# Kernel tuning notes

Measured on AMD Instinct MI355X. Metric: run time of the kernel, lower is better.

The kernel has to match this reference:

```python
import jax, jax.numpy as jnp
import numpy as np

N_HEADS = 8
EPS = 1e-5


def setup_inputs() -> dict:
    key = jax.random.key(0)
    ks = jax.random.split(key, 5)
    c = 512
    x = jax.random.normal(ks[0], (2, c, 2, 32, 32), dtype=jnp.float32)
    s = 0.02
    Wq = jax.random.normal(ks[1], (c, c), dtype=jnp.float32) * s
    Wk = jax.random.normal(ks[2], (c, c), dtype=jnp.float32) * s
    Wv = jax.random.normal(ks[3], (c, c), dtype=jnp.float32) * s
    Wo = jax.random.normal(ks[4], (c, c), dtype=jnp.float32) * s
    bo = jnp.zeros((c,), dtype=jnp.float32)
    gamma = jnp.ones((c,), dtype=jnp.float32)
    beta = jnp.zeros((c,), dtype=jnp.float32)
    return {"x": x, "Wq": Wq, "Wk": Wk, "Wv": Wv, "Wo": Wo, "bo": bo,
            "gamma": gamma, "beta": beta}


def reference(x, Wq, Wk, Wv, Wo, bo, gamma, beta):
    b, c, d, h, w = x.shape
    seq = d * h * w
    # [b, c, d, h, w] -> [b, seq, c]
    xs = jnp.transpose(x, (0, 2, 3, 4, 1)).reshape(b, seq, c)
    # LayerNorm over channel dim
    mu = jnp.mean(xs, axis=-1, keepdims=True)
    var = jnp.mean(jnp.square(xs - mu), axis=-1, keepdims=True)
    xn = (xs - mu) * jax.lax.rsqrt(var + EPS) * gamma + beta
    # Self-attention (cond falls back to x); weights stored [in, out]
    dh = c // N_HEADS
    q = (xn @ Wq).reshape(b, seq, N_HEADS, dh)
    k = (xn @ Wk).reshape(b, seq, N_HEADS, dh)
    v = (xn @ Wv).reshape(b, seq, N_HEADS, dh)
    scale = dh ** (-0.5)
    attn = jnp.einsum('bihd,bjhd->bhij', q, k) * scale  # [b, H, seq, seq]
    attn = jax.nn.softmax(attn, axis=-1)
    out = jnp.einsum('bhij,bjhd->bihd', attn, v).reshape(b, seq, c)
    out = out @ Wo + bo
    y = out + xs  # residual
    return jnp.transpose(y.reshape(b, d, h, w, c), (0, 4, 1, 2, 3))
```

## Files before the change

### kernel.cpp

```cpp
#include <hip/hip_runtime.h>
#include <cstdint>
#include <cstring>

typedef unsigned short u16;
typedef unsigned char u8;
typedef __bf16 bf16x8 __attribute__((ext_vector_type(8)));
typedef float f32x4 __attribute__((ext_vector_type(4)));
typedef u16 u16x4 __attribute__((ext_vector_type(4)));
typedef u16 u16x8 __attribute__((ext_vector_type(8)));
typedef long l64x2 __attribute__((ext_vector_type(2)));

__device__ __forceinline__ u16 f2bf(float f) {
  union { float f; unsigned u; } v; v.f = f;
  unsigned r = v.u + 0x7FFFu + ((v.u >> 16) & 1u);
  return (u16)(r >> 16);
}

__device__ __forceinline__ float bf2f(u16 u) {
  union { unsigned u; float f; } c; c.u = ((unsigned)u) << 16;
  return c.f;
}

__device__ __forceinline__ f32x4 mfma16(bf16x8 a, bf16x8 b, f32x4 c) {
  return __builtin_amdgcn_mfma_f32_16x16x32_bf16(a, b, c, 0, 0, 0);
}

__device__ __forceinline__ f32x4 mfma8(long a, long b, f32x4 c) {
  return __builtin_amdgcn_mfma_f32_16x16x32_fp8_fp8(a, b, c, 0, 0, 0);
}

__device__ __forceinline__ u8 f2fp8(float f) {
  return (u8)(__builtin_amdgcn_cvt_pk_fp8_f32(f, f, 0, false) & 0xff);
}

__device__ __forceinline__ void gload_lds16(const void* g, void* l) {
  auto* lp = reinterpret_cast<__attribute__((address_space(3))) unsigned int*>(
      reinterpret_cast<uintptr_t>(l));
  const auto* gp = reinterpret_cast<const __attribute__((address_space(1))) unsigned int*>(
      reinterpret_cast<uintptr_t>(g));
  __builtin_amdgcn_global_load_lds(gp, lp, 16, 0, 0);
}

template <int N>
__device__ __forceinline__ void waitcnt_vm() {
  if constexpr (N == 0)      asm volatile("s_waitcnt vmcnt(0)" ::: "memory");
  else if constexpr (N == 2) asm volatile("s_waitcnt vmcnt(2)" ::: "memory");
  else if constexpr (N == 4) asm volatile("s_waitcnt vmcnt(4)" ::: "memory");
  else if constexpr (N == 6) asm volatile("s_waitcnt vmcnt(6)" ::: "memory");
  else                       asm volatile("s_waitcnt vmcnt(8)" ::: "memory");
}

__global__ __launch_bounds__(256) void prep_kernel(const float* __restrict__ Wq,
                                                   const float* __restrict__ Wk,
                                                   const float* __restrict__ Wv,
                                                   const float* __restrict__ Wo,
                                                   const float* __restrict__ x,
                                                   const float* __restrict__ gamma,
                                                   const float* __restrict__ beta,
                                                   u8* __restrict__ wt8f,
                                                   u16* __restrict__ wtWo,
                                                   u8* __restrict__ xn8f) {
  struct LnSh {
    float red0[16][16];
    float red1[16][16];
    float mu[16], rs[16];
    u8 tile8[16][520];
  };
  struct WtSh { float tile[32][33]; };
  __shared__ __align__(16) char shraw[sizeof(LnSh) > sizeof(WtSh) ? sizeof(LnSh) : sizeof(WtSh)];
  int bid = blockIdx.x;
  int t = threadIdx.x;
  if (bid < 256) {
    LnSh& S = *reinterpret_cast<LnSh*>(shraw);
    int b = bid >> 7;
    int s0 = (bid & 127) * 16;
    int tx = t & 15, ty = t >> 4;
    const float* xb = x + (size_t)b * 512 * 2048 + s0 + tx;
    float vals[32];
    float sum = 0.f, sq = 0.f;
#pragma unroll
    for (int k = 0; k < 32; k++) {
      float v = xb[(size_t)(ty + k * 16) * 2048];
      vals[k] = v;
      sum += v; sq += v * v;
    }
    S.red0[ty][tx] = sum; S.red1[ty][tx] = sq;
    __syncthreads();
    if (t < 16) {
      float a = 0.f, c2 = 0.f;
#pragma unroll
      for (int i = 0; i < 16; i++) { a += S.red0[i][t]; c2 += S.red1[i][t]; }
      float mu = a * (1.f / 512.f);
      float var = c2 * (1.f / 512.f) - mu * mu;
      S.mu[t] = mu;
      S.rs[t] = rsqrtf(var + 1e-5f);
    }
    __syncthreads();
    float mu = S.mu[tx], rs = S.rs[tx];
#pragma unroll
    for (int k = 0; k < 32; k++) {
      int ch = ty + k * 16;
      S.tile8[tx][ch] = f2fp8((vals[k] - mu) * rs * gamma[ch] + beta[ch]);
    }
    __syncthreads();
    int lrow2 = t & 15, kt = t >> 4;
    int grow = b * 2048 + s0;
    int rt2 = grow >> 5;
    int ihalf = (s0 >> 4) & 1;
    u8* dst = xn8f + ((size_t)rt2 * 16 + kt) * 1024 + ihalf * 8;
#pragma unroll
    for (int kg = 0; kg < 4; kg++) {
      unsigned long long v;
      memcpy(&v, &S.tile8[lrow2][kt * 32 + kg * 8], 8);
      *(unsigned long long*)(dst + (size_t)(lrow2 + kg * 16) * 16) = v;
    }
  } else {
    WtSh& S = *reinterpret_cast<WtSh*>(shraw);
    int wid = bid - 256;
    int z = wid >> 8;
    const float* W = (z == 0) ? Wq : (z == 1) ? Wk : (z == 2) ? Wv : Wo;
    int rem = wid & 255;
    int n0 = (rem >> 4) * 32, k0 = (rem & 15) * 32;
    int tx = t & 31, ty = t >> 5;
#pragma unroll
    for (int i = 0; i < 4; i++)
      S.tile[ty + i * 8][tx] = W[(size_t)(k0 + ty + i * 8) * 512 + n0 + tx];
    __syncthreads();
    if (z < 3) {
      if (t < 128) {
        int lane = t >> 1, jhalf = t & 1;
        int nn = (lane & 15) + jhalf * 16;
        int kk0 = (lane >> 4) * 8;
        u8 pk[8];
#pragma unroll
        for (int j = 0; j < 8; j++) pk[j] = f2fp8(S.tile[kk0 + j][nn]);
        unsigned long long v;
        memcpy(&v, pk, 8);
        size_t addr = (size_t)z * 262144 + ((size_t)(n0 >> 5) * 16 + (k0 >> 5)) * 1024 +
                      (size_t)lane * 16 + jhalf * 8;
        *(unsigned long long*)(wt8f + addr) = v;
      }
    } else {
#pragma unroll
      for (int i = 0; i < 4; i++) {
        int n = ty + i * 8;
        wtWo[(size_t)(n0 + n) * 512 + k0 + tx] = f2bf(S.tile[tx][n]);
      }
    }
  }
}

template <int AM, int AN>
__device__ __forceinline__ void gemm_tile_ring(const u16* __restrict__ A, const u16* __restrict__ B,
                                               int m0, int n0, f32x4 acc[AM][AN],
                                               u16* As, u16* Bs) {
  constexpr int BM = AM * 32, BN = AN * 32;
  constexpr int LA = BM / 64, LB = BN / 64;
  constexpr int L = LA + LB;
  int t = threadIdx.x;
  int w = t >> 6, lane = t & 63;
  int wm = w >> 1, wn = w & 1;
  int arow = t >> 2;
  int acol = (t & 3) * 8;
  int lrow = lane & 15;
  int lko = (lane >> 4) * 8;

  auto stage = [&](int buf, int k0) {
#pragma unroll
    for (int g = 0; g < LA; ++g)
      gload_lds16(A + (size_t)(m0 + g * 64 + arow) * 512 + k0 + acol,
                  As + buf * (BM * 32) + g * 2048 + w * 512);
#pragma unroll
    for (int g = 0; g < LB; ++g)
      gload_lds16(B + (size_t)(n0 + g * 64 + arow) * 512 + k0 + acol,
                  Bs + buf * (BN * 32) + g * 2048 + w * 512);
  };

  stage(0, 0);
  stage(1, 32);
  stage(2, 64);
  __syncthreads();

  for (int tt = 0; tt < 16; ++tt) {
    int pk = (tt + 3 < 16) ? (tt + 3) * 32 : 0;
    stage((tt + 3) & 3, pk);
    const u16* as = As + (tt & 3) * (BM * 32);
    const u16* bs = Bs + (tt & 3) * (BN * 32);
    bf16x8 af[AM], bfr[AN];
#pragma unroll
    for (int i = 0; i < AM; i++) af[i] = *(const bf16x8*)(as + (wm * (AM * 16) + i * 16 + lrow) * 32 + lko);
#pragma unroll
    for (int j = 0; j < AN; j++) bfr[j] = *(const bf16x8*)(bs + (wn * (AN * 16) + j * 16 + lrow) * 32 + lko);
    __builtin_amdgcn_s_setprio(1);
#pragma unroll
    for (int i = 0; i < AM; i++)
#pragma unroll
      for (int j = 0; j < AN; j++)
        acc[i][j] = mfma16(af[i], bfr[j], acc[i][j]);
    __builtin_amdgcn_s_setprio(0);
    waitcnt_vm<2 * L>();
    __builtin_amdgcn_s_barrier();
  }
  waitcnt_vm<0>();
}

__global__ __launch_bounds__(256, 4) void gemm_qkv(const u8* __restrict__ xn8f, const u8* __restrict__ wt8f,
                                                   u8* __restrict__ Qb, u8* __restrict__ Kp,
                                                   u8* __restrict__ Vp) {
  const float SCQ = 0.125f * 1.4426950408889634f;
  int mat = blockIdx.z;
  int bx = blockIdx.x, by = blockIdx.y;
  int t = threadIdx.x, w = t >> 6, lane = t & 63;
  int lrow = lane & 15, lgrp = lane >> 4;

  const u8* Af = xn8f + (size_t)(bx * 4 + w) * 16384 + (size_t)lane * 16;
  const u8* Bf = wt8f + (size_t)mat * 262144 + (size_t)(by * 2) * 16384 + (size_t)lane * 16;

  f32x4 acc[2][4] = {};
  long aA[2], bA[4], aB[2], bB[4];

  auto loadAB = [&](long* a, long* bb, int kt) {
    l64x2 av = *(const l64x2*)(Af + kt * 1024);
    l64x2 b0 = *(const l64x2*)(Bf + kt * 1024);
    l64x2 b1 = *(const l64x2*)(Bf + 16384 + kt * 1024);
    a[0] = av[0]; a[1] = av[1];
    bb[0] = b0[0]; bb[1] = b0[1]; bb[2] = b1[0]; bb[3] = b1[1];
  };
  auto step = [&](const long* a, const long* bb) {
    __builtin_amdgcn_s_setprio(1);
#pragma unroll
    for (int i = 0; i < 2; i++)
#pragma unroll
      for (int j = 0; j < 4; j++)
        acc[i][j] = mfma8(a[i], bb[j], acc[i][j]);
    __builtin_amdgcn_s_setprio(0);
  };

  loadAB(aA, bA, 0);
  for (int kt = 0; kt < 16; kt += 2) {
    loadAB(aB, bB, (kt + 1) & 15);
    step(aA, bA);
    loadAB(aA, bA, (kt + 2) & 15);
    step(aB, bB);
  }

#pragma unroll
  for (int i = 0; i < 2; i++) {
#pragma unroll
    for (int j = 0; j < 4; j++) {
      int gr0 = bx * 128 + w * 32 + i * 16 + lgrp * 4;
      int gc = by * 64 + j * 16 + lrow;
      if (mat == 0) {
#pragma unroll
        for (int r = 0; r < 4; r++)
          Qb[(size_t)(gr0 + r) * 512 + gc] = f2fp8(acc[i][j][r] * SCQ);
      } else if (mat == 1) {
        int h = gc >> 6, d = gc & 63;
        int half = d >> 5, lg = (d >> 3) & 3, jj = d & 7;
#pragma unroll
        for (int r = 0; r < 4; r++) {
          int kg = gr0 + r;
          int bq = kg >> 11, kl = kg & 2047;
          int kt2 = kl >> 5, kw = kl & 31;
          int tt = (kw >> 2) & 1;
          int kwb = kw - 4 * tt;
          int lr = ((kwb >> 3) << 2) | (kwb & 3);
          size_t idx = (size_t)((bq * 8 + h) * 64 + kt2) * 2048 + tt * 1024 +
                       (lg * 16 + lr) * 16 + half * 8 + jj;
          Kp[idx] = f2fp8(acc[i][j][r]);
        }
      } else {
        int h = gc >> 6, d = gc & 63;
        int dt = d >> 4, lr = d & 15;
        int kg = gr0;
        int bq = kg >> 11, kl = kg & 2047;
        int kt2 = kl >> 5, kw = kl & 31;
        int lg = kw >> 3, j0 = kw & 7;
        unsigned u = __builtin_amdgcn_cvt_pk_fp8_f32(acc[i][j][0], acc[i][j][1], 0, false);
        u = __builtin_amdgcn_cvt_pk_fp8_f32(acc[i][j][2], acc[i][j][3], u, true);
        size_t idx = (size_t)((bq * 8 + h) * 64 + kt2) * 2048 + (dt >> 1) * 1024 +
                     (lg * 16 + lr) * 16 + (dt & 1) * 8 + j0;
        *(unsigned*)(Vp + idx) = u;
      }
    }
  }
}

__global__ __launch_bounds__(256, 4) void attn_kernel(const u8* __restrict__ Qb, const u8* __restrict__ Kp,
                                                      const u8* __restrict__ Vp, u16* __restrict__ Opart,
                                                      float* __restrict__ ml, int logS) {
  const long ONES8 = 0x3838383838383838L;
  int S = 1 << logS;
  int bid = blockIdx.x;
  int qt = bid >> (4 + logS);
  int group = bid & (16 * S - 1);
  int hb = group >> logS, sp = group & (S - 1);
  int b = hb >> 3, h = hb & 7;
  int kt0 = sp * (64 >> logS);
  int nsteps = 64 >> logS;

  int t = threadIdx.x, w = t >> 6, lane = t & 63;
  int lrow = lane & 15, lgrp = lane >> 4, lko = lgrp * 8;
  int q0 = qt * 128 + w * 32;

  const u8* Qp = Qb + (size_t)(b * 2048 + q0 + lrow) * 512 + h * 64 + lko;
  long qa0 = *(const long*)(Qp);
  long qa1 = *(const long*)(Qp + 32);
  long qb0 = *(const long*)(Qp + 16 * 512);
  long qb1 = *(const long*)(Qp + 16 * 512 + 32);

  const u8* Kbh = Kp + (size_t)hb * 131072 + lane * 16;
  const u8* Vbh = Vp + (size_t)hb * 131072 + lane * 16;

  f32x4 acca[4] = {}, accb[4] = {};
  f32x4 suma = {}, sumb = {};

  long kA[4], vA[4], kB[4], vB[4];

  auto loadKV = [&](long* kf, long* vf, int st) {
    const u8* pk = Kbh + (size_t)(kt0 + st) * 2048;
    const u8* pv = Vbh + (size_t)(kt0 + st) * 2048;
    l64x2 a0 = *(const l64x2*)(pk);
    l64x2 a1 = *(const l64x2*)(pk + 1024);
    l64x2 b0 = *(const l64x2*)(pv);
    l64x2 b1 = *(const l64x2*)(pv + 1024);
    kf[0] = a0[0]; kf[1] = a0[1]; kf[2] = a1[0]; kf[3] = a1[1];
    vf[0] = b0[0]; vf[1] = b0[1]; vf[2] = b1[0]; vf[3] = b1[1];
  };

  auto computeStep = [&](const long* kc, const long* vc) {
    f32x4 sa0 = {}, sa1 = {}, sb0 = {}, sb1 = {};
    __builtin_amdgcn_s_setprio(1);
    sa0 = mfma8(kc[0], qa0, sa0);
    sa0 = mfma8(kc[1], qa1, sa0);
    sa1 = mfma8(kc[2], qa0, sa1);
    sa1 = mfma8(kc[3], qa1, sa1);
    sb0 = mfma8(kc[0], qb0, sb0);
    sb0 = mfma8(kc[1], qb1, sb0);
    sb1 = mfma8(kc[2], qb0, sb1);
    sb1 = mfma8(kc[3], qb1, sb1);
    __builtin_amdgcn_s_setprio(0);

    float pa[8], pb8[8];
#pragma unroll
    for (int jj = 0; jj < 4; jj++) pa[jj] = exp2f(sa0[jj]);
#pragma unroll
    for (int jj = 0; jj < 4; jj++) pa[4 + jj] = exp2f(sa1[jj]);
#pragma unroll
    for (int jj = 0; jj < 4; jj++) pb8[jj] = exp2f(sb0[jj]);
#pragma unroll
    for (int jj = 0; jj < 4; jj++) pb8[4 + jj] = exp2f(sb1[jj]);

    unsigned alo = __builtin_amdgcn_cvt_pk_fp8_f32(pa[0], pa[1], 0, false);
    alo = __builtin_amdgcn_cvt_pk_fp8_f32(pa[2], pa[3], alo, true);
    unsigned ahi = __builtin_amdgcn_cvt_pk_fp8_f32(pa[4], pa[5], 0, false);
    ahi = __builtin_amdgcn_cvt_pk_fp8_f32(pa[6], pa[7], ahi, true);
    long pla = (long)(((unsigned long long)ahi << 32) | alo);
    unsigned blo = __builtin_amdgcn_cvt_pk_fp8_f32(pb8[0], pb8[1], 0, false);
    blo = __builtin_amdgcn_cvt_pk_fp8_f32(pb8[2], pb8[3], blo, true);
    unsigned bhi = __builtin_amdgcn_cvt_pk_fp8_f32(pb8[4], pb8[5], 0, false);
    bhi = __builtin_amdgcn_cvt_pk_fp8_f32(pb8[6], pb8[7], bhi, true);
    long plb = (long)(((unsigned long long)bhi << 32) | blo);

    __builtin_amdgcn_s_setprio(1);
    acca[0] = mfma8(pla, vc[0], acca[0]);
    acca[1] = mfma8(pla, vc[1], acca[1]);
    acca[2] = mfma8(pla, vc[2], acca[2]);
    acca[3] = mfma8(pla, vc[3], acca[3]);
    accb[0] = mfma8(plb, vc[0], accb[0]);
    accb[1] = mfma8(plb, vc[1], accb[1]);
    accb[2] = mfma8(plb, vc[2], accb[2]);
    accb[3] = mfma8(plb, vc[3], accb[3]);
    suma = mfma8(pla, ONES8, suma);
    sumb = mfma8(plb, ONES8, sumb);
    __builtin_amdgcn_s_setprio(0);
  };

  loadKV(kA, vA, 0);
  for (int st = 0; st < nsteps; st += 2) {
    loadKV(kB, vB, (st + 1 < nsteps) ? st + 1 : 0);
    computeStep(kA, vA);
    loadKV(kA, vA, (st + 2 < nsteps) ? st + 2 : 0);
    computeStep(kB, vB);
  }

  if (lrow == 0) {
    int rowa = b * 2048 + q0 + lgrp * 4;
#pragma unroll
    for (int r = 0; r < 4; r++) {
      ml[(size_t)sp * 32768 + (rowa + r) * 8 + h] = suma[r];
      ml[(size_t)sp * 32768 + (rowa + 16 + r) * 8 + h] = sumb[r];
    }
  }

  u16* Ao = Opart + (size_t)sp * 2097152 + (size_t)(b * 2048 + q0) * 512 + h * 64;
#pragma unroll
  for (int r = 0; r < 4; r++) {
#pragma unroll
    for (int dt = 0; dt < 4; dt++) {
      Ao[(size_t)(lgrp * 4 + r) * 512 + dt * 16 + lrow] = f2bf(acca[dt][r]);
      Ao[(size_t)(16 + lgrp * 4 + r) * 512 + dt * 16 + lrow] = f2bf(accb[dt][r]);
    }
  }
}

template <int S>
__global__ __launch_bounds__(256) void attn_combine(const u16* __restrict__ Opart,
                                                    const float* __restrict__ ml,
                                                    u16* __restrict__ AO) {
  int gid = blockIdx.x * 256 + threadIdx.x;
  int pair = gid >> 3, dcol = (gid & 7) * 8;
  int row = pair >> 3, h = pair & 7;
  float lsum = 0.f;
#pragma unroll
  for (int s = 0; s < S; s++) lsum += ml[(size_t)s * 32768 + pair];
  float inv = 1.0f / lsum;
  float o[8] = {};
#pragma unroll
  for (int s = 0; s < S; s++) {
    u16x8 ov = *(const u16x8*)(Opart + (size_t)s * 2097152 + (size_t)row * 512 + h * 64 + dcol);
#pragma unroll
    for (int j = 0; j < 8; j++) o[j] += bf2f(ov[j]);
  }
  u16x8 outv;
#pragma unroll
  for (int j = 0; j < 8; j++) outv[j] = f2bf(o[j] * inv);
  *(u16x8*)(AO + (size_t)row * 512 + h * 64 + dcol) = outv;
}

__global__ __launch_bounds__(256) void gemm_out(const u16* __restrict__ AO, const u16* __restrict__ WoT,
                                                const float* __restrict__ bo, const float* __restrict__ x,
                                                float* __restrict__ y) {
  __shared__ u16 As[4 * 64 * 32];
  __shared__ u16 Bs[4 * 64 * 32];
  int m0 = blockIdx.x * 64, n0 = blockIdx.y * 64;
  f32x4 acc[2][2] = {};
  gemm_tile_ring<2, 2>(AO, WoT, m0, n0, acc, As, Bs);
  int t = threadIdx.x, w = t >> 6, lane = t & 63;
  int wm = w >> 1, wn = w & 1, lrow = lane & 15, lgrp = lane >> 4;
#pragma unroll
  for (int i = 0; i < 2; i++) {
#pragma unroll
    for (int j = 0; j < 2; j++) {
      int gr0 = m0 + wm * 32 + i * 16 + lgrp * 4;
      int gc = n0 + wn * 32 + j * 16 + lrow;
      int bb = gr0 >> 11, s = gr0 & 2047;
      float bias = bo[gc];
      const float* xp = x + ((size_t)bb * 512 + gc) * 2048 + s;
      float4 xv = *(const float4*)xp;
      float4 o;
      o.x = acc[i][j][0] + bias + xv.x;
      o.y = acc[i][j][1] + bias + xv.y;
      o.z = acc[i][j][2] + bias + xv.z;
      o.w = acc[i][j][3] + bias + xv.w;
      *(float4*)(y + ((size_t)bb * 512 + gc) * 2048 + s) = o;
    }
  }
}

extern "C" void kernel_launch(void* const* d_in, const int* in_sizes, int n_in,
                              void* d_out, int out_size, void* d_ws, size_t ws_size,
                              hipStream_t stream) {
  const float* x = (const float*)d_in[0];
  const float* Wq = (const float*)d_in[1];
  const float* Wk = (const float*)d_in[2];
  const float* Wv = (const float*)d_in[3];
  const float* Wo = (const float*)d_in[4];
  const float* bo = (const float*)d_in[5];
  const float* gamma = (const float*)d_in[6];
  const float* beta = (const float*)d_in[7];
  float* y = (float*)d_out;
  char* ws = (char*)d_ws;
  u8* xn8f = (u8*)(ws);
  u8* wt8f = (u8*)(ws + (2 << 20));
  u16* wtWo = (u16*)(ws + (3 << 20));
  u8* Qb = (u8*)(ws + (4 << 20));
  u8* Kp = (u8*)(ws + (6 << 20));
  u8* Vp = (u8*)(ws + (8 << 20));
  u16* AO = (u16*)(ws + (10 << 20));
  float* ml = (float*)(ws + (14 << 20));
  u16* Opart = (u16*)(ws + (15 << 20));

  int logS;
  if (ws_size >= (40u << 20)) logS = 2;
  else if (ws_size >= (32u << 20)) logS = 1;
  else { logS = 0; Opart = AO; }

  prep_kernel<<<dim3(1280), dim3(256), 0, stream>>>(Wq, Wk, Wv, Wo, x, gamma, beta, wt8f, wtWo, xn8f);
  gemm_qkv<<<dim3(32, 8, 3), dim3(256), 0, stream>>>(xn8f, wt8f, Qb, Kp, Vp);
  attn_kernel<<<dim3(256 << logS), dim3(256), 0, stream>>>(Qb, Kp, Vp, Opart, ml, logS);
  if (logS == 2)      attn_combine<4><<<dim3(1024), dim3(256), 0, stream>>>(Opart, ml, AO);
  else if (logS == 1) attn_combine<2><<<dim3(1024), dim3(256), 0, stream>>>(Opart, ml, AO);
  else                attn_combine<1><<<dim3(1024), dim3(256), 0, stream>>>(Opart, ml, AO);
  gemm_out<<<dim3(64, 8), dim3(256), 0, stream>>>(AO, wtWo, bo, x, y);
}
```

Baseline: 57.57 us.

## Run output projection in FP8 with pre-swizzled fragment layout

The output projection now uses FP8 MFMA instead of a bf16 LDS-ring GEMM. Wo is quantized in the prep kernel into the same fragment-packed layout as Wq/Wk/Wv, and attn_combine writes the attention output directly as packed FP8 fragments. gemm_out_f8 then loads operands straight from global memory into registers with double buffering, skipping LDS. This halves operand bytes and the cost of the MFMA stage, at the price of extra quantization error on the attention output and Wo. The workspace layout is compacted, so the split-K thresholds change.

```diff
diff --git a/kernel.cpp b/kernel.cpp
--- a/kernel.cpp
+++ b/kernel.cpp
@@ -6,7 +6,6 @@
 typedef unsigned char u8;
 typedef __bf16 bf16x8 __attribute__((ext_vector_type(8)));
 typedef float f32x4 __attribute__((ext_vector_type(4)));
-typedef u16 u16x4 __attribute__((ext_vector_type(4)));
 typedef u16 u16x8 __attribute__((ext_vector_type(8)));
 typedef long l64x2 __attribute__((ext_vector_type(2)));
 
@@ -21,33 +20,12 @@
   return c.f;
 }
 
-__device__ __forceinline__ f32x4 mfma16(bf16x8 a, bf16x8 b, f32x4 c) {
-  return __builtin_amdgcn_mfma_f32_16x16x32_bf16(a, b, c, 0, 0, 0);
-}
-
 __device__ __forceinline__ f32x4 mfma8(long a, long b, f32x4 c) {
   return __builtin_amdgcn_mfma_f32_16x16x32_fp8_fp8(a, b, c, 0, 0, 0);
 }
 
 __device__ __forceinline__ u8 f2fp8(float f) {
   return (u8)(__builtin_amdgcn_cvt_pk_fp8_f32(f, f, 0, false) & 0xff);
-}
-
-__device__ __forceinline__ void gload_lds16(const void* g, void* l) {
-  auto* lp = reinterpret_cast<__attribute__((address_space(3))) unsigned int*>(
-      reinterpret_cast<uintptr_t>(l));
-  const auto* gp = reinterpret_cast<const __attribute__((address_space(1))) unsigned int*>(
-      reinterpret_cast<uintptr_t>(g));
-  __builtin_amdgcn_global_load_lds(gp, lp, 16, 0, 0);
-}
-
-template <int N>
-__device__ __forceinline__ void waitcnt_vm() {
-  if constexpr (N == 0)      asm volatile("s_waitcnt vmcnt(0)" ::: "memory");
-  else if constexpr (N == 2) asm volatile("s_waitcnt vmcnt(2)" ::: "memory");
-  else if constexpr (N == 4) asm volatile("s_waitcnt vmcnt(4)" ::: "memory");
-  else if constexpr (N == 6) asm volatile("s_waitcnt vmcnt(6)" ::: "memory");
-  else                       asm volatile("s_waitcnt vmcnt(8)" ::: "memory");
 }
 
 __global__ __launch_bounds__(256) void prep_kernel(const float* __restrict__ Wq,
@@ -58,7 +36,6 @@
                                                    const float* __restrict__ gamma,
                                                    const float* __restrict__ beta,
                                                    u8* __restrict__ wt8f,
-                                                   u16* __restrict__ wtWo,
                                                    u8* __restrict__ xn8f) {
   struct LnSh {
     float red0[16][16];
@@ -126,82 +103,20 @@
     for (int i = 0; i < 4; i++)
       S.tile[ty + i * 8][tx] = W[(size_t)(k0 + ty + i * 8) * 512 + n0 + tx];
     __syncthreads();
-    if (z < 3) {
-      if (t < 128) {
-        int lane = t >> 1, jhalf = t & 1;
-        int nn = (lane & 15) + jhalf * 16;
-        int kk0 = (lane >> 4) * 8;
-        u8 pk[8];
-#pragma unroll
-        for (int j = 0; j < 8; j++) pk[j] = f2fp8(S.tile[kk0 + j][nn]);
-        unsigned long long v;
-        memcpy(&v, pk, 8);
-        size_t addr = (size_t)z * 262144 + ((size_t)(n0 >> 5) * 16 + (k0 >> 5)) * 1024 +
-                      (size_t)lane * 16 + jhalf * 8;
-        *(unsigned long long*)(wt8f + addr) = v;
-      }
-    } else {
-#pragma unroll
-      for (int i = 0; i < 4; i++) {
-        int n = ty + i * 8;
-        wtWo[(size_t)(n0 + n) * 512 + k0 + tx] = f2bf(S.tile[tx][n]);
-      }
-    }
-  }
-}
-
-template <int AM, int AN>
-__device__ __forceinline__ void gemm_tile_ring(const u16* __restrict__ A, const u16* __restrict__ B,
-                                               int m0, int n0, f32x4 acc[AM][AN],
-                                               u16* As, u16* Bs) {
-  constexpr int BM = AM * 32, BN = AN * 32;
-  constexpr int LA = BM / 64, LB = BN / 64;
-  constexpr int L = LA + LB;
-  int t = threadIdx.x;
-  int w = t >> 6, lane = t & 63;
-  int wm = w >> 1, wn = w & 1;
-  int arow = t >> 2;
-  int acol = (t & 3) * 8;
-  int lrow = lane & 15;
-  int lko = (lane >> 4) * 8;
-
-  auto stage = [&](int buf, int k0) {
-#pragma unroll
-    for (int g = 0; g < LA; ++g)
-      gload_lds16(A + (size_t)(m0 + g * 64 + arow) * 512 + k0 + acol,
-                  As + buf * (BM * 32) + g * 2048 + w * 512);
-#pragma unroll
-    for (int g = 0; g < LB; ++g)
-      gload_lds16(B + (size_t)(n0 + g * 64 + arow) * 512 + k0 + acol,
-                  Bs + buf * (BN * 32) + g * 2048 + w * 512);
-  };
-
-  stage(0, 0);
-  stage(1, 32);
-  stage(2, 64);
-  __syncthreads();
-
-  for (int tt = 0; tt < 16; ++tt) {
-    int pk = (tt + 3 < 16) ? (tt + 3) * 32 : 0;
-    stage((tt + 3) & 3, pk);
-    const u16* as = As + (tt & 3) * (BM * 32);
-    const u16* bs = Bs + (tt & 3) * (BN * 32);
-    bf16x8 af[AM], bfr[AN];
-#pragma unroll
-    for (int i = 0; i < AM; i++) af[i] = *(const bf16x8*)(as + (wm * (AM * 16) + i * 16 + lrow) * 32 + lko);
-#pragma unroll
-    for (int j = 0; j < AN; j++) bfr[j] = *(const bf16x8*)(bs + (wn * (AN * 16) + j * 16 + lrow) * 32 + lko);
-    __builtin_amdgcn_s_setprio(1);
-#pragma unroll
-    for (int i = 0; i < AM; i++)
-#pragma unroll
-      for (int j = 0; j < AN; j++)
-        acc[i][j] = mfma16(af[i], bfr[j], acc[i][j]);
-    __builtin_amdgcn_s_setprio(0);
-    waitcnt_vm<2 * L>();
-    __builtin_amdgcn_s_barrier();
-  }
-  waitcnt_vm<0>();
+    if (t < 128) {
+      int lane = t >> 1, jhalf = t & 1;
+      int nn = (lane & 15) + jhalf * 16;
+      int kk0 = (lane >> 4) * 8;
+      u8 pk[8];
+#pragma unroll
+      for (int j = 0; j < 8; j++) pk[j] = f2fp8(S.tile[kk0 + j][nn]);
+      unsigned long long v;
+      memcpy(&v, pk, 8);
+      size_t addr = (size_t)z * 262144 + ((size_t)(n0 >> 5) * 16 + (k0 >> 5)) * 1024 +
+                    (size_t)lane * 16 + jhalf * 8;
+      *(unsigned long long*)(wt8f + addr) = v;
+    }
+  }
 }
 
 __global__ __launch_bounds__(256, 4) void gemm_qkv(const u8* __restrict__ xn8f, const u8* __restrict__ wt8f,
@@ -407,7 +322,7 @@
 template <int S>
 __global__ __launch_bounds__(256) void attn_combine(const u16* __restrict__ Opart,
                                                     const float* __restrict__ ml,
-                                                    u16* __restrict__ AO) {
+                                                    u8* __restrict__ AOf) {
   int gid = blockIdx.x * 256 + threadIdx.x;
   int pair = gid >> 3, dcol = (gid & 7) * 8;
   int row = pair >> 3, h = pair & 7;
@@ -422,28 +337,61 @@
 #pragma unroll
     for (int j = 0; j < 8; j++) o[j] += bf2f(ov[j]);
   }
-  u16x8 outv;
-#pragma unroll
-  for (int j = 0; j < 8; j++) outv[j] = f2bf(o[j] * inv);
-  *(u16x8*)(AO + (size_t)row * 512 + h * 64 + dcol) = outv;
-}
-
-__global__ __launch_bounds__(256) void gemm_out(const u16* __restrict__ AO, const u16* __restrict__ WoT,
-                                                const float* __restrict__ bo, const float* __restrict__ x,
-                                                float* __restrict__ y) {
-  __shared__ u16 As[4 * 64 * 32];
-  __shared__ u16 Bs[4 * 64 * 32];
-  int m0 = blockIdx.x * 64, n0 = blockIdx.y * 64;
-  f32x4 acc[2][2] = {};
-  gemm_tile_ring<2, 2>(AO, WoT, m0, n0, acc, As, Bs);
+  unsigned lo = __builtin_amdgcn_cvt_pk_fp8_f32(o[0] * inv, o[1] * inv, 0, false);
+  lo = __builtin_amdgcn_cvt_pk_fp8_f32(o[2] * inv, o[3] * inv, lo, true);
+  unsigned hi = __builtin_amdgcn_cvt_pk_fp8_f32(o[4] * inv, o[5] * inv, 0, false);
+  hi = __builtin_amdgcn_cvt_pk_fp8_f32(o[6] * inv, o[7] * inv, hi, true);
+  unsigned long long v = ((unsigned long long)hi << 32) | lo;
+  int col = h * 64 + dcol;
+  size_t addr = ((size_t)(row >> 5) * 16 + (col >> 5)) * 1024 +
+                ((size_t)((row & 15) + ((col >> 3) & 3) * 16)) * 16 + ((row >> 4) & 1) * 8;
+  *(unsigned long long*)(AOf + addr) = v;
+}
+
+__global__ __launch_bounds__(256, 4) void gemm_out_f8(const u8* __restrict__ AOf, const u8* __restrict__ wt8f,
+                                                      const float* __restrict__ bo, const float* __restrict__ x,
+                                                      float* __restrict__ y) {
+  int bx = blockIdx.x, by = blockIdx.y;
   int t = threadIdx.x, w = t >> 6, lane = t & 63;
-  int wm = w >> 1, wn = w & 1, lrow = lane & 15, lgrp = lane >> 4;
+  int lrow = lane & 15, lgrp = lane >> 4;
+
+  const u8* Af = AOf + (size_t)(bx * 4 + w) * 16384 + (size_t)lane * 16;
+  const u8* Bf = wt8f + (size_t)3 * 262144 + (size_t)(by * 2) * 16384 + (size_t)lane * 16;
+
+  f32x4 acc[2][4] = {};
+  long aA[2], bA[4], aB[2], bB[4];
+
+  auto loadAB = [&](long* a, long* bb, int kt) {
+    l64x2 av = *(const l64x2*)(Af + kt * 1024);
+    l64x2 b0 = *(const l64x2*)(Bf + kt * 1024);
+    l64x2 b1 = *(const l64x2*)(Bf + 16384 + kt * 1024);
+    a[0] = av[0]; a[1] = av[1];
+    bb[0] = b0[0]; bb[1] = b0[1]; bb[2] = b1[0]; bb[3] = b1[1];
+  };
+  auto step = [&](const long* a, const long* bb) {
+    __builtin_amdgcn_s_setprio(1);
+#pragma unroll
+    for (int i = 0; i < 2; i++)
+#pragma unroll
+      for (int j = 0; j < 4; j++)
+        acc[i][j] = mfma8(a[i], bb[j], acc[i][j]);
+    __builtin_amdgcn_s_setprio(0);
+  };
+
+  loadAB(aA, bA, 0);
+  for (int kt = 0; kt < 16; kt += 2) {
+    loadAB(aB, bB, (kt + 1) & 15);
+    step(aA, bA);
+    loadAB(aA, bA, (kt + 2) & 15);
+    step(aB, bB);
+  }
+
 #pragma unroll
   for (int i = 0; i < 2; i++) {
 #pragma unroll
-    for (int j = 0; j < 2; j++) {
-      int gr0 = m0 + wm * 32 + i * 16 + lgrp * 4;
-      int gc = n0 + wn * 32 + j * 16 + lrow;
+    for (int j = 0; j < 4; j++) {
+      int gr0 = bx * 128 + w * 32 + i * 16 + lgrp * 4;
+      int gc = by * 64 + j * 16 + lrow;
       int bb = gr0 >> 11, s = gr0 & 2047;
       float bias = bo[gc];
       const float* xp = x + ((size_t)bb * 512 + gc) * 2048 + s;
@@ -473,24 +421,23 @@
   char* ws = (char*)d_ws;
   u8* xn8f = (u8*)(ws);
   u8* wt8f = (u8*)(ws + (2 << 20));
-  u16* wtWo = (u16*)(ws + (3 << 20));
-  u8* Qb = (u8*)(ws + (4 << 20));
-  u8* Kp = (u8*)(ws + (6 << 20));
-  u8* Vp = (u8*)(ws + (8 << 20));
-  u16* AO = (u16*)(ws + (10 << 20));
-  float* ml = (float*)(ws + (14 << 20));
-  u16* Opart = (u16*)(ws + (15 << 20));
+  u8* Qb = (u8*)(ws + (3 << 20));
+  u8* Kp = (u8*)(ws + (5 << 20));
+  u8* Vp = (u8*)(ws + (7 << 20));
+  u8* AOf = (u8*)(ws + (9 << 20));
+  float* ml = (float*)(ws + (11 << 20));
+  u16* Opart = (u16*)(ws + (12 << 20));
 
   int logS;
-  if (ws_size >= (40u << 20)) logS = 2;
-  else if (ws_size >= (32u << 20)) logS = 1;
-  else { logS = 0; Opart = AO; }
-
-  prep_kernel<<<dim3(1280), dim3(256), 0, stream>>>(Wq, Wk, Wv, Wo, x, gamma, beta, wt8f, wtWo, xn8f);
+  if (ws_size >= (28u << 20)) logS = 2;
+  else if (ws_size >= (20u << 20)) logS = 1;
+  else logS = 0;
+
+  prep_kernel<<<dim3(1280), dim3(256), 0, stream>>>(Wq, Wk, Wv, Wo, x, gamma, beta, wt8f, xn8f);
   gemm_qkv<<<dim3(32, 8, 3), dim3(256), 0, stream>>>(xn8f, wt8f, Qb, Kp, Vp);
   attn_kernel<<<dim3(256 << logS), dim3(256), 0, stream>>>(Qb, Kp, Vp, Opart, ml, logS);
-  if (logS == 2)      attn_combine<4><<<dim3(1024), dim3(256), 0, stream>>>(Opart, ml, AO);
-  else if (logS == 1) attn_combine<2><<<dim3(1024), dim3(256), 0, stream>>>(Opart, ml, AO);
-  else                attn_combine<1><<<dim3(1024), dim3(256), 0, stream>>>(Opart, ml, AO);
-  gemm_out<<<dim3(64, 8), dim3(256), 0, stream>>>(AO, wtWo, bo, x, y);
-}
+  if (logS == 2)      attn_combine<4><<<dim3(1024), dim3(256), 0, stream>>>(Opart, ml, AOf);
+  else if (logS == 1) attn_combine<2><<<dim3(1024), dim3(256), 0, stream>>>(Opart, ml, AOf);
+  else                attn_combine<1><<<dim3(1024), dim3(256), 0, stream>>>(Opart, ml, AOf);
+  gemm_out_f8<<<dim3(32, 8), dim3(256), 0, stream>>>(AOf, wt8f, bo, x, y);
+}
```

Measured after the change: 57.28 us. Within noise of the previous version (-0.5%).
